# Kernel optimization log

Measured on AMD Instinct MI355X. Metric: run time of the kernel, lower is better.

Reference implementation:

```python
import jax, jax.numpy as jnp
import numpy as np

B, T, F = 32, 1024, 64
H = 128          # num_lstm_out
KH = 16          # kan_hidden_dim
C1, C2, C3 = 128, 256, 128
NC = 10


def _glorot(key, shape):
    fan_in = shape[0] if len(shape) == 2 else int(np.prod(shape[1:]))
    return (jax.random.normal(key, shape, jnp.float32) / np.sqrt(fan_in)).astype(jnp.float32)


def setup_inputs() -> dict:
    key = jax.random.key(0)
    ks = jax.random.split(key, 24)
    D = F + H
    d = {}
    d['x'] = jax.random.normal(ks[0], (B, T, F), jnp.float32)
    d['eps_z'] = jax.random.normal(ks[1], (B, H), jnp.float32)
    d['eps_cat'] = jax.random.normal(ks[2], (B, H), jnp.float32)
    # KAN-LSTM cell: gates = W2 @ silu(W1 @ [x;h])
    d['kan_w1'] = _glorot(ks[3], (D, KH)); d['kan_b1'] = jnp.zeros((KH,), jnp.float32)
    d['kan_w2'] = _glorot(ks[4], (KH, 4 * H)); d['kan_b2'] = jnp.zeros((4 * H,), jnp.float32)
    # causal convs (OIH layout)
    d['conv1_w'] = _glorot(ks[5], (C1, F, 8)); d['conv1_b'] = jnp.zeros((C1,), jnp.float32)
    d['conv2_w'] = _glorot(ks[6], (C2, C1, 5)); d['conv2_b'] = jnp.zeros((C2,), jnp.float32)
    d['conv3_w'] = _glorot(ks[7], (C3, C2, 3)); d['conv3_b'] = jnp.zeros((C3,), jnp.float32)
    # batchnorm affine params
    d['bn1_g'] = jnp.ones((C1,), jnp.float32); d['bn1_b'] = jnp.zeros((C1,), jnp.float32)
    d['bn2_g'] = jnp.ones((C2,), jnp.float32); d['bn2_b'] = jnp.zeros((C2,), jnp.float32)
    d['bn3_g'] = jnp.ones((C3,), jnp.float32); d['bn3_b'] = jnp.zeros((C3,), jnp.float32)
    # SE layers (reduction=16, no bias)
    d['se1_w1'] = _glorot(ks[8], (C1, C1 // 16)); d['se1_w2'] = _glorot(ks[9], (C1 // 16, C1))
    d['se2_w1'] = _glorot(ks[10], (C2, C2 // 16)); d['se2_w2'] = _glorot(ks[11], (C2 // 16, C2))
    # VIB heads
    d['fc_mu_w'] = _glorot(ks[12], (H, H)); d['fc_mu_b'] = jnp.zeros((H,), jnp.float32)
    d['fc_std_w'] = _glorot(ks[13], (H, H)); d['fc_std_b'] = jnp.zeros((H,), jnp.float32)
    d['fc_mu_cat_w'] = _glorot(ks[14], (2 * H, H)); d['fc_mu_cat_b'] = jnp.zeros((H,), jnp.float32)
    d['fc_std_cat_w'] = _glorot(ks[15], (2 * H, H)); d['fc_std_cat_b'] = jnp.zeros((H,), jnp.float32)
    d['fc_w'] = _glorot(ks[16], (H + C3, NC)); d['fc_b'] = jnp.zeros((NC,), jnp.float32)
    return d


def _kan_lstm(x, w1, b1, w2, b2):
    # x: (B,T,F) -> hidden (B,T,H); sequential recurrence via lax.scan
    xT = jnp.swapaxes(x, 0, 1)  # (T,B,F)
    h0 = jnp.zeros((x.shape[0], H), x.dtype)
    c0 = jnp.zeros((x.shape[0], H), x.dtype)

    def step(carry, xt):
        h, c = carry
        g = jax.nn.silu(jnp.concatenate([xt, h], axis=-1) @ w1 + b1) @ w2 + b2  # (B,4H)
        i_, f_, g_, o_ = jnp.split(g, 4, axis=-1)
        c = jax.nn.sigmoid(f_) * c + jax.nn.sigmoid(i_) * jnp.tanh(g_)
        h = jax.nn.sigmoid(o_) * jnp.tanh(c)
        return (h, c), h

    _, hs = jax.lax.scan(step, (h0, c0), xT)
    return jnp.swapaxes(hs, 0, 1)  # (B,T,H)


def _cluster_hidden(hidden):
    # hidden: (B,T,H). Pairwise cosine sim -> exp kernel -> best 2-block cut.
    Tn = hidden.shape[1]
    last = hidden[:, -1, :]
    hn = hidden / jnp.clip(jnp.linalg.norm(hidden, axis=-1, keepdims=True), 1e-8)
    S = jnp.exp(-5.5 * (1.0 - jnp.einsum('bik,bjk->bij', hn, hn)))  # (B,T,T)
    S = S * (1.0 - jnp.eye(Tn, dtype=S.dtype))  # zero diagonal
    # 2D prefix sums give all block sums in O(T^2) instead of O(T^3)
    P = jnp.cumsum(jnp.cumsum(S, axis=1), axis=2)
    i = jnp.arange(1, Tn)
    TL = P[:, i - 1, i - 1]                 # (B,T-1) sum of [:i,:i]
    full = P[:, -1, -1][:, None]
    TR = P[:, i - 1, -1] - TL               # sum of [:i,i:]
    BL = P[:, -1, i - 1] - TL               # sum of [i:,:i]
    BR = full - TL - TR - BL                # sum of [i:,i:]
    ii = i.astype(S.dtype)
    nn = (Tn - i).astype(S.dtype)
    dist = TL / (ii * ii) + BR / (nn * nn) - (TR + BL) / (ii * nn)
    cuts = jnp.argmax(dist, axis=1) + 1     # (B,)
    mask = (jnp.arange(Tn)[None, :] < cuts[:, None]).astype(hidden.dtype)
    corr = jnp.einsum('bt,bth->bh', mask, hidden) / cuts[:, None].astype(hidden.dtype)
    return last, corr


def _causal_conv(x, w, b):
    k = w.shape[-1]
    xp = jnp.pad(x, ((0, 0), (0, 0), (k - 1, 0)))
    y = jax.lax.conv_general_dilated(xp, w, (1,), 'VALID',
                                     dimension_numbers=('NCH', 'OIH', 'NCH'))
    return y + b[None, :, None]


def _bn(x, g, b, eps=1e-3):
    m = x.mean(axis=(0, 2), keepdims=True)
    v = x.var(axis=(0, 2), keepdims=True)
    return (x - m) / jnp.sqrt(v + eps) * g[None, :, None] + b[None, :, None]


def _se(x, w1, w2):
    y = x.mean(axis=2)                       # (B,C)
    y = jax.nn.sigmoid(jax.nn.relu(y @ w1) @ w2)
    return x * y[:, :, None]


def reference(x, eps_z, eps_cat, kan_w1, kan_b1, kan_w2, kan_b2,
              conv1_w, conv1_b, conv2_w, conv2_b, conv3_w, conv3_b,
              bn1_g, bn1_b, bn2_g, bn2_b, bn3_g, bn3_b,
              se1_w1, se1_w2, se2_w1, se2_w2,
              fc_mu_w, fc_mu_b, fc_std_w, fc_std_b,
              fc_mu_cat_w, fc_mu_cat_b, fc_std_cat_w, fc_std_cat_b,
              fc_w, fc_b):
    # LSTM branch
    hidden = _kan_lstm(x, kan_w1, kan_b1, kan_w2, kan_b2)      # (B,T,H)
    out, corr = _cluster_hidden(hidden)
    mu = corr @ fc_mu_w + fc_mu_b
    std = jax.nn.softplus(corr @ fc_std_w + fc_std_b)
    z = mu + std * eps_z
    xz = jnp.concatenate([out, z], axis=1)                      # (B,2H)
    mu_cat = xz @ fc_mu_cat_w + fc_mu_cat_b
    std_cat = jax.nn.softplus(xz @ fc_std_cat_w + fc_std_cat_b)
    x1 = mu_cat + std_cat * eps_cat   # dropout in eval mode = identity
    # FCN branch
    x2 = jnp.swapaxes(x, 1, 2)                                  # (B,F,T)
    x2 = jax.nn.gelu(_bn(_causal_conv(x2, conv1_w, conv1_b), bn1_g, bn1_b), approximate=False)
    x2 = _se(x2, se1_w1, se1_w2)
    x2 = jax.nn.gelu(_bn(_causal_conv(x2, conv2_w, conv2_b), bn2_g, bn2_b), approximate=False)
    x2 = _se(x2, se2_w1, se2_w2)
    x2 = jax.nn.gelu(_bn(_causal_conv(x2, conv3_w, conv3_b), bn3_g, bn3_b), approximate=False)
    x2 = x2.mean(axis=2)                                        # (B,C3)
    x_all = jnp.concatenate([x1, x2], axis=1)
    logits = x_all @ fc_w + fc_b
    return (jax.nn.log_softmax(logits, axis=1), mu, std, mu_cat, std_cat)
```

## Files before the change

kernel.cpp:

```cpp
#include <hip/hip_runtime.h>
#include <math.h>

#define B_ 32
#define T_ 1024
#define F_ 64
#define H_ 128
#define D_ 192
#define KH_ 16
#define C1_ 128
#define C2_ 256
#define C3_ 128
#define NC_ 10

typedef float v2f __attribute__((ext_vector_type(2)));
typedef float f32x4 __attribute__((ext_vector_type(4)));
typedef __bf16 bfrag __attribute__((ext_vector_type(8)));

__device__ __forceinline__ float sig_(float x){ return 1.f/(1.f+__expf(-x)); }
__device__ __forceinline__ float tanh_(float x){ return 1.f - 2.f/(__expf(2.f*x)+1.f); }
__device__ __forceinline__ float gelu_(float x){ return 0.5f*x*(1.f+erff(x*0.70710678118654752f)); }
__device__ __forceinline__ float softplus_(float x){ return fmaxf(x,0.f) + log1pf(__expf(-fabsf(x))); }

__device__ __forceinline__ unsigned bfpack(float a, float b){
  unsigned ua = __float_as_uint(a), ub = __float_as_uint(b);
  ua = ua + 0x7FFFu + ((ua>>16)&1u);
  ub = ub + 0x7FFFu + ((ub>>16)&1u);
  return (ua>>16) | (ub & 0xFFFF0000u);
}
__device__ __forceinline__ unsigned short bf1(float a){
  unsigned ua = __float_as_uint(a);
  ua = ua + 0x7FFFu + ((ua>>16)&1u);
  return (unsigned short)(ua>>16);
}
__device__ __forceinline__ float bf2f(unsigned short h){
  return __uint_as_float(((unsigned)h)<<16);
}

#define QPERM_XOR1(x) __int_as_float(__builtin_amdgcn_mov_dpp(__float_as_int(x), 0xB1, 0xF, 0xF, true))
#define QPERM_XOR2(x) __int_as_float(__builtin_amdgcn_mov_dpp(__float_as_int(x), 0x4E, 0xF, 0xF, true))

#define LDS_BARRIER() asm volatile("s_waitcnt lgkmcnt(0)\n\ts_barrier" ::: "memory")


__device__ __forceinline__ void ax_body(int blk, char* smemraw,
    const float* __restrict__ x, const float* __restrict__ w1, const float* __restrict__ b1,
    float* __restrict__ axT)
{
  struct AxS { float xs[16][68]; float w1s[64][16]; };
  AxS* sm = (AxS*)smemraw;
  const int bt0 = blk*16;
  const int tid = threadIdx.x;
  for(int i=tid;i<64*16;i+=256){ sm->w1s[i>>4][i&15] = w1[i]; }
  for(int i=tid;i<16*64;i+=256){ const int r=i>>6, d=i&63; sm->xs[r][d] = x[(size_t)(bt0+r)*64 + d]; }
  __syncthreads();
  const int r = tid>>4, j = tid&15;
  float s = b1[j];
  #pragma unroll
  for(int d=0; d<64; d++) s += sm->xs[r][d]*sm->w1s[d][j];
  const int bt = bt0 + r;
  axT[((size_t)(bt>>10)*16 + j)*1024 + (bt&1023)] = s;
}

__device__ __forceinline__ void prepack_body(int blk,
    const float* __restrict__ w1s, const float* __restrict__ w2s, const float* __restrict__ w3s,
    unsigned short* __restrict__ wp1, unsigned short* __restrict__ wp2, unsigned short* __restrict__ wp3)
{
  int e = blk*256 + threadIdx.x;
  if(e >= 65536+163840+98304) return;
  const float* w; unsigned short* wp; int Cout, Cin, Kw;
  if(e < 65536){ w=w1s; wp=wp1; Cout=C1_; Cin=F_;  Kw=8; }
  else if(e < 65536+163840){ e-=65536; w=w2s; wp=wp2; Cout=C2_; Cin=C1_; Kw=5; }
  else { e-=229376; w=w3s; wp=wp3; Cout=C3_; Cin=C2_; Kw=3; }
  const int co = e/(Cin*Kw);
  const int rem = e - co*(Cin*Kw);
  const int ci = rem/Kw, kw = rem - ci*Kw;
  const int off = (((ci>>5)*Kw + kw)*(Cout>>4) + (co>>4))*512 + ((co&15)*4 + ((ci>>3)&3))*8 + (ci&7);
  wp[off] = bf1(w[e]);
}

__device__ __forceinline__ void norm_body(int blk,
    const float* __restrict__ hidden,
    unsigned short* __restrict__ hnhi, unsigned short* __restrict__ hnlo)
{
  const int row = blk*8 + (threadIdx.x>>5);
  const int l = threadIdx.x&31;
  const float* hr = hidden + (size_t)row*H_;
  float s = 0.f;
  for(int k=l;k<H_;k+=32){ float v=hr[k]; s+=v*v; }
  #pragma unroll
  for(int m=16;m>=1;m>>=1) s += __shfl_xor(s, m, 64);
  const float inv = 1.f/fmaxf(sqrtf(s), 1e-8f);
  const float4 v = *(const float4*)&hr[l*4];
  const float f0=v.x*inv, f1=v.y*inv, f2=v.z*inv, f3=v.w*inv;
  const unsigned short h0=bf1(f0), h1=bf1(f1), h2=bf1(f2), h3=bf1(f3);
  uint2 phi; phi.x = (unsigned)h0 | ((unsigned)h1<<16); phi.y = (unsigned)h2 | ((unsigned)h3<<16);
  *(uint2*)&hnhi[(size_t)row*H_ + l*4] = phi;
  const unsigned short g0=bf1(f0-bf2f(h0)), g1=bf1(f1-bf2f(h1)), g2=bf1(f2-bf2f(h2)), g3=bf1(f3-bf2f(h3));
  uint2 plo; plo.x = (unsigned)g0 | ((unsigned)g1<<16); plo.y = (unsigned)g2 | ((unsigned)g3<<16);
  *(uint2*)&hnlo[(size_t)row*H_ + l*4] = plo;
}

struct SS {
  unsigned short Ahi[64*136];
  unsigned short Alo[64*136];
  unsigned short Bhi[64*136];
  unsigned short Blo[64*136];
  double red[64][17];
};
__device__ __forceinline__ void s_body(int blk, char* smemraw,
    const unsigned short* __restrict__ hnhi, const unsigned short* __restrict__ hnlo,
    double* __restrict__ rowsum, double* __restrict__ psum)
{
  SS* sm = (SS*)smemraw;
  const int b = blk >> 4;
  const int i0 = (blk & 15) * 64;
  const int tid = threadIdx.x, l = tid & 63, wv = tid >> 6;
  const int m = l & 15, q = l >> 4;

  {
    const uint4* ghi = (const uint4*)(hnhi + ((size_t)b*T_ + i0)*H_);
    const uint4* glo = (const uint4*)(hnlo + ((size_t)b*T_ + i0)*H_);
    for(int idx=tid; idx<64*16; idx+=256){
      const int r = idx>>4, c8 = idx&15;
      *(uint4*)&sm->Ahi[r*136 + c8*8] = ghi[r*16 + c8];
      *(uint4*)&sm->Alo[r*136 + c8*8] = glo[r*16 + c8];
    }
  }

  double rs[4]={0,0,0,0}, ps[4]={0,0,0,0};
  const int arow = (wv*16 + m)*136;

  for(int jt=0;jt<16;jt++){
    const int j0 = jt*64;
    __syncthreads();
    {
      const uint4* ghi = (const uint4*)(hnhi + ((size_t)b*T_ + j0)*H_);
      const uint4* glo = (const uint4*)(hnlo + ((size_t)b*T_ + j0)*H_);
      for(int idx=tid; idx<64*16; idx+=256){
        const int r = idx>>4, c8 = idx&15;
        *(uint4*)&sm->Bhi[r*136 + c8*8] = ghi[r*16 + c8];
        *(uint4*)&sm->Blo[r*136 + c8*8] = glo[r*16 + c8];
      }
    }
    __syncthreads();

    f32x4 acc[4];
    #pragma unroll
    for(int nt=0;nt<4;nt++) acc[nt] = (f32x4)(0.f);
    #pragma unroll
    for(int kc=0;kc<4;kc++){
      const bfrag Ah = *(const bfrag*)&sm->Ahi[arow + kc*32 + q*8];
      const bfrag Al = *(const bfrag*)&sm->Alo[arow + kc*32 + q*8];
      #pragma unroll
      for(int nt=0;nt<4;nt++){
        const int brow = (nt*16 + m)*136 + kc*32 + q*8;
        const bfrag Bh = *(const bfrag*)&sm->Bhi[brow];
        const bfrag Bl = *(const bfrag*)&sm->Blo[brow];
        acc[nt] = __builtin_amdgcn_mfma_f32_16x16x32_bf16(Ah, Bh, acc[nt], 0, 0, 0);
        acc[nt] = __builtin_amdgcn_mfma_f32_16x16x32_bf16(Al, Bh, acc[nt], 0, 0, 0);
        acc[nt] = __builtin_amdgcn_mfma_f32_16x16x32_bf16(Ah, Bl, acc[nt], 0, 0, 0);
      }
    }
    #pragma unroll
    for(int nt=0;nt<4;nt++){
      const int gj = j0 + nt*16 + m;
      #pragma unroll
      for(int r=0;r<4;r++){
        const int gi = i0 + wv*16 + q*4 + r;
        if(gi == gj) continue;
        const float sv = __expf(-5.5f*(1.f - acc[nt][r]));
        rs[r] += (double)sv;
        if(gj < gi) ps[r] += (double)sv;
      }
    }
  }
  __syncthreads();
  #pragma unroll
  for(int r=0;r<4;r++) sm->red[wv*16 + q*4 + r][m] = rs[r];
  __syncthreads();
  if(tid<64){ double v=0; for(int k=0;k<16;k++) v+=sm->red[tid][k]; rowsum[(size_t)b*T_ + i0 + tid]=v; }
  __syncthreads();
  #pragma unroll
  for(int r=0;r<4;r++) sm->red[wv*16 + q*4 + r][m] = ps[r];
  __syncthreads();
  if(tid<64){ double v=0; for(int k=0;k<16;k++) v+=sm->red[tid][k]; psum[(size_t)b*T_ + i0 + tid]=v; }
}

struct CS {
  double sr[256]; double sp[256]; double bd[256]; double totR;
  float c2[2][128]; int bidx[256]; int cut;
};
__device__ __forceinline__ void cluster_body(int b, char* smemraw,
    const double* __restrict__ rowsum, const double* __restrict__ psum,
    const float* __restrict__ hidden, float* __restrict__ corr, int* __restrict__ cuts)
{
  CS* sm = (CS*)smemraw;
  const int tid = threadIdx.x;
  const double* r = rowsum + (size_t)b*T_;
  const double* p = psum + (size_t)b*T_;
  double r4[4], p4[4];
  #pragma unroll
  for(int q=0;q<4;q++){ r4[q]=r[tid*4+q]; p4[q]=p[tid*4+q]; }
  sm->sr[tid]=r4[0]+r4[1]+r4[2]+r4[3];
  sm->sp[tid]=p4[0]+p4[1]+p4[2]+p4[3];
  __syncthreads();
  if(tid==0){
    double ar=0, ap=0;
    for(int i=0;i<256;i++){ double tr=sm->sr[i], tp=sm->sp[i]; sm->sr[i]=ar; sm->sp[i]=ap; ar+=tr; ap+=tp; }
    sm->totR = ar;
  }
  __syncthreads();
  double cr = sm->sr[tid], cp = sm->sp[tid];
  const double full = sm->totR;
  double best = -1e308; int bi = 1;
  #pragma unroll
  for(int q=0;q<4;q++){
    cr += r4[q]; cp += p4[q];
    const int i = 4*tid + q + 1;
    if(i < T_){
      const double TL = 2.0*cp;
      const double TRv = cr - TL;
      const double BR = full - TL - 2.0*TRv;
      const double di = (double)i, dn = (double)(T_-i);
      const double dist = TL/(di*di) + BR/(dn*dn) - (2.0*TRv)/(di*dn);
      if(dist > best){ best=dist; bi=i; }
    }
  }
  sm->bd[tid]=best; sm->bidx[tid]=bi;
  __syncthreads();
  if(tid==0){
    double bb=-1e308; int ii=1;
    for(int q=0;q<256;q++){ if(sm->bd[q]>bb){ bb=sm->bd[q]; ii=sm->bidx[q]; } }
    sm->cut=ii; cuts[b]=ii;
  }
  __syncthreads();
  const int cut = sm->cut;
  const int h = tid&127, half = tid>>7;
  float s=0.f;
  const float* hb = hidden + (size_t)b*T_*H_;
  #pragma unroll 4
  for(int t=half; t<cut; t+=2) s += hb[(size_t)t*H_ + h];
  sm->c2[half][h]=s;
  __syncthreads();
  if(tid<128) corr[b*H_+tid] = (sm->c2[0][tid]+sm->c2[1][tid])/(float)cut;
}

__device__ __forceinline__ void head1_body(int b, char* smemraw,
    const float* __restrict__ corr, const float* __restrict__ hidden,
    const float* __restrict__ eps_z, const float* __restrict__ eps_cat,
    const float* __restrict__ mu_w, const float* __restrict__ mu_b,
    const float* __restrict__ std_w, const float* __restrict__ std_b,
    const float* __restrict__ muc_w, const float* __restrict__ muc_b,
    const float* __restrict__ stdc_w, const float* __restrict__ stdc_b,
    float* __restrict__ out_mu, float* __restrict__ out_std,
    float* __restrict__ out_muc, float* __restrict__ out_stdc, float* __restrict__ x1)
{
  struct H1 { float cs[128]; float xz[256]; };
  H1* sm = (H1*)smemraw;
  const int h = threadIdx.x;
  if(h<128){
    sm->cs[h]=corr[b*H_+h];
    sm->xz[h]=hidden[((size_t)b*T_ + (T_-1))*H_ + h];
  }
  __syncthreads();
  if(h<128){
    float m=mu_b[h], sdv=std_b[h];
    for(int k=0;k<H_;k++){ const float cv=sm->cs[k]; m+=cv*mu_w[k*H_+h]; sdv+=cv*std_w[k*H_+h]; }
    const float stdv = softplus_(sdv);
    out_mu[b*H_+h]=m; out_std[b*H_+h]=stdv;
    sm->xz[128+h] = m + stdv*eps_z[b*H_+h];
  }
  __syncthreads();
  if(h<128){
    float mc=muc_b[h], sc=stdc_b[h];
    for(int k=0;k<256;k++){ const float v=sm->xz[k]; mc+=v*muc_w[k*H_+h]; sc+=v*stdc_w[k*H_+h]; }
    const float stdc = softplus_(sc);
    out_muc[b*H_+h]=mc; out_stdc[b*H_+h]=stdc;
    x1[b*H_+h]=mc + stdc*eps_cat[b*H_+h];
  }
}

struct ConvS {
  float sescale[256];
  float seh[16];
  unsigned short xs[72*40];
};
__device__ __forceinline__ void conv_body(int bx, int by, int bz, char* smemraw,
    const float* __restrict__ in, const unsigned short* __restrict__ wp,
    const float* __restrict__ bias,
    const float* __restrict__ se_in, const float* __restrict__ se_w1,
    const float* __restrict__ se_w2, int seR,
    float* __restrict__ y, float* __restrict__ bnacc, int Cin, int Cout, int Kw)
{
  ConvS* sm = (ConvS*)smemraw;
  unsigned short* xs = sm->xs;
  const int b = bz, t0 = bx*64, co0 = by*64;
  const int tid = threadIdx.x, l = tid&63, wv = tid>>6;
  const int q = l>>4, m = l&15;
  const int TW = 64 + Kw - 1;
  const int abase = (wv*16 + m)*40 + q*8;
  const int boff = (m*4 + q)*8;
  const bool use_se = (se_in != nullptr);

  if(use_se){
    float* ms = (float*)xs;
    if(tid<Cin) ms[tid] = se_in[b*Cin+tid] * (1.f/(float)T_);
    __syncthreads();
    if(tid<seR){ float s=0.f; for(int k=0;k<Cin;k++) s += ms[k]*se_w1[k*seR+tid]; sm->seh[tid]=fmaxf(s,0.f); }
    __syncthreads();
    if(tid<Cin){ float s=0.f; for(int k=0;k<seR;k++) s += sm->seh[k]*se_w2[k*Cin+tid]; sm->sescale[tid]=sig_(s); }
  }

  f32x4 acc[4];
  #pragma unroll
  for(int nt=0;nt<4;nt++) acc[nt] = (f32x4)(0.f);

  const int nchunks = Cin >> 5;
  for(int cc=0; cc<nchunks; cc++){
    __syncthreads();
    for(int idx=tid; idx<TW*8; idx+=256){
      const int r = idx>>3, c4 = (idx&7)*4;
      const int tg = t0 - (Kw-1) + r;
      uint2 pk = make_uint2(0u, 0u);
      if(tg >= 0){
        float4 v = *(const float4*)&in[((size_t)b*T_ + tg)*Cin + cc*32 + c4];
        if(use_se){
          const float4 s4 = *(const float4*)&sm->sescale[cc*32 + c4];
          v.x*=s4.x; v.y*=s4.y; v.z*=s4.z; v.w*=s4.w;
        }
        pk.x = bfpack(v.x, v.y); pk.y = bfpack(v.z, v.w);
      }
      *(uint2*)&xs[r*40 + c4] = pk;
    }
    __syncthreads();
    for(int kw=0; kw<Kw; kw++){
      const bfrag Af = *(const bfrag*)&xs[abase + kw*40];
      #pragma unroll
      for(int nt=0; nt<4; nt++){
        const unsigned short* wpp = wp + ((size_t)((cc*Kw + kw)*(Cout>>4) + (by*4 + nt)))*512 + boff;
        const bfrag Bf = *(const bfrag*)wpp;
        acc[nt] = __builtin_amdgcn_mfma_f32_16x16x32_bf16(Af, Bf, acc[nt], 0, 0, 0);
      }
    }
  }
  __syncthreads();
  float* part = (float*)xs;
  const int t_base = t0 + wv*16 + q*4;
  #pragma unroll
  for(int nt=0; nt<4; nt++){
    const int co = co0 + nt*16 + m;
    const float bv = bias[co];
    float s1 = 0.f, s2 = 0.f;
    #pragma unroll
    for(int r=0;r<4;r++){
      const float v = acc[nt][r] + bv;
      y[((size_t)b*T_ + t_base + r)*Cout + co] = v;
      s1 += v; s2 += v*v;
    }
    s1 += __shfl_xor(s1, 16); s1 += __shfl_xor(s1, 32);
    s2 += __shfl_xor(s2, 16); s2 += __shfl_xor(s2, 32);
    if(q==0){ part[(wv*64 + nt*16 + m)*2+0] = s1; part[(wv*64 + nt*16 + m)*2+1] = s2; }
  }
  __syncthreads();
  if(tid < 64){
    float a1=0.f, a2=0.f;
    #pragma unroll
    for(int w2i=0; w2i<4; w2i++){ a1 += part[(w2i*64+tid)*2+0]; a2 += part[(w2i*64+tid)*2+1]; }
    atomicAdd(&bnacc[co0 + tid], a1);
    atomicAdd(&bnacc[Cout + co0 + tid], a2);
  }
}

__device__ __forceinline__ void bn_act_body(int b, int chunk, char* smemraw,
    float* __restrict__ y, const float* __restrict__ bnacc,
    const float* __restrict__ gw, const float* __restrict__ bw,
    float* __restrict__ mean_acc, int C, int write_y)
{
  const int t0 = chunk*128, tid = threadIdx.x;
  const int c = tid & (C-1), part = tid / C, np = 256 / C;
  const float cnt = (float)(B_*T_);
  const float mm = bnacc[c]/cnt;
  const float var = bnacc[C+c]/cnt - mm*mm;
  const float sc = gw[c]/sqrtf(var+1e-3f);
  const float sh = bw[c] - mm*sc;
  float s = 0.f;
  for(int t=t0+part; t<t0+128; t+=np){
    const size_t off = ((size_t)b*T_ + t)*C + c;
    float v = y[off];
    v = gelu_(v*sc + sh);
    if(write_y) y[off] = v;
    s += v;
  }
  float* rs = (float*)smemraw;
  if(np > 1){
    rs[tid]=s;
    __syncthreads();
    if(part==0) s += rs[tid+C];
  }
  if(part==0) atomicAdd(&mean_acc[b*C+c], s);
}

__device__ __forceinline__ void lstm_seg_body(int b, int ts, int nsteps, char* smemraw,
    const float* __restrict__ axT, const float* __restrict__ w1,
    const float* __restrict__ w2, const float* __restrict__ b2,
    float* __restrict__ hidden, float* __restrict__ cstate)
{
  float (*hs)[148] = (float(*)[148])smemraw;
  const int tid = threadIdx.x;
  const int l = tid & 63, wv = tid >> 6;
  const int j = l >> 2, g = l & 3;
  const int hi = wv*64 + l;

  v2f w1hv[16];
  #pragma unroll
  for(int q=0;q<16;q++){
    w1hv[q].x = w1[(64 + g*32 + 2*q)*KH_ + j];
    w1hv[q].y = w1[(64 + g*32 + 2*q + 1)*KH_ + j];
  }
  v2f w2if[16], w2go[16];
  #pragma unroll
  for(int k=0;k<16;k++){
    w2if[k].x = w2[k*512 + hi];       w2if[k].y = w2[k*512 + 128 + hi];
    w2go[k].x = w2[k*512 + 256 + hi]; w2go[k].y = w2[k*512 + 384 + hi];
  }
  v2f bif, bgo;
  bif.x = b2[hi]; bif.y = b2[128+hi]; bgo.x = b2[256+hi]; bgo.y = b2[384+hi];

  const float* axr = axT + ((size_t)b*16 + j)*1024;
  float* hb = hidden + (size_t)b*T_*H_;
  const int hwi = (hi>>5)*36 + (hi&31);
  float c;
  if(ts == 0){
    for(int i=tid;i<2*148;i+=128) ((float*)hs)[i]=0.f;
    c = 0.f;
  } else {
    c = cstate[b*H_ + hi];
    hs[0][hwi] = hb[(size_t)(ts-1)*H_ + hi];
  }
  float4 axA = *(const float4*)&axr[ts];
  float4 axB = *(const float4*)&axr[ts+4];
  __syncthreads();

#define LSTM_STEP(tt, axv, RB) { \
    const float* hsr = hs[RB]; \
    float* hsw = hs[1-(RB)]; \
    v2f ap0=(v2f)(0.f), ap1=(v2f)(0.f), ap2=(v2f)(0.f), ap3=(v2f)(0.f); \
    { const float4 hv = *(const float4*)&hsr[g*36 + 0];  ap0 += ((v2f){hv.x,hv.y})*w1hv[0]  + ((v2f){hv.z,hv.w})*w1hv[1]; } \
    { const float4 hv = *(const float4*)&hsr[g*36 + 4];  ap1 += ((v2f){hv.x,hv.y})*w1hv[2]  + ((v2f){hv.z,hv.w})*w1hv[3]; } \
    { const float4 hv = *(const float4*)&hsr[g*36 + 8];  ap2 += ((v2f){hv.x,hv.y})*w1hv[4]  + ((v2f){hv.z,hv.w})*w1hv[5]; } \
    { const float4 hv = *(const float4*)&hsr[g*36 + 12]; ap3 += ((v2f){hv.x,hv.y})*w1hv[6]  + ((v2f){hv.z,hv.w})*w1hv[7]; } \
    { const float4 hv = *(const float4*)&hsr[g*36 + 16]; ap0 += ((v2f){hv.x,hv.y})*w1hv[8]  + ((v2f){hv.z,hv.w})*w1hv[9]; } \
    { const float4 hv = *(const float4*)&hsr[g*36 + 20]; ap1 += ((v2f){hv.x,hv.y})*w1hv[10] + ((v2f){hv.z,hv.w})*w1hv[11]; } \
    { const float4 hv = *(const float4*)&hsr[g*36 + 24]; ap2 += ((v2f){hv.x,hv.y})*w1hv[12] + ((v2f){hv.z,hv.w})*w1hv[13]; } \
    { const float4 hv = *(const float4*)&hsr[g*36 + 28]; ap3 += ((v2f){hv.x,hv.y})*w1hv[14] + ((v2f){hv.z,hv.w})*w1hv[15]; } \
    const v2f apt = (ap0+ap1)+(ap2+ap3); \
    float a = apt.x + apt.y; \
    a += QPERM_XOR1(a); \
    a += QPERM_XOR2(a); \
    a += (axv); \
    const float g1 = a * sig_(a); \
    v2f aIF = bif, aGO = bgo; \
    _Pragma("unroll") \
    for(int k=0;k<16;k++){ \
      const float gk = __int_as_float(__builtin_amdgcn_readlane(__float_as_int(g1), 4*k)); \
      v2f gk2; gk2.x=gk; gk2.y=gk; \
      aIF += gk2 * w2if[k]; \
      aGO += gk2 * w2go[k]; \
    } \
    const float si = sig_(aIF.x); \
    const float sf = sig_(aIF.y); \
    const float tg = tanh_(aGO.x); \
    const float so = sig_(aGO.y); \
    c = sf*c + si*tg; \
    const float h = so * tanh_(c); \
    hsw[hwi] = h; \
    hb[(size_t)(tt)*H_ + hi] = h; \
    LDS_BARRIER(); \
  }

  const int te = ts + nsteps;
  for(int t0=ts;t0<te;t0+=4){
    const int tl = (t0+8 < 1020) ? (t0+8) : 1020;
    const float4 axC = *(const float4*)&axr[tl];
    LSTM_STEP(t0+0, axA.x, 0)
    LSTM_STEP(t0+1, axA.y, 1)
    LSTM_STEP(t0+2, axA.z, 0)
    LSTM_STEP(t0+3, axA.w, 1)
    axA = axB; axB = axC;
  }
#undef LSTM_STEP
  if(te < T_) cstate[b*H_ + hi] = c;
}


__global__ __launch_bounds__(256) void mega0_kernel(
    const float* c1w, const float* c2w, const float* c3w,
    unsigned short* wp1, unsigned short* wp2, unsigned short* wp3,
    const float* x, const float* kw1, const float* kb1, float* axT)
{
  __shared__ __align__(16) char sm[16*68*4 + 64*16*4];
  const int bid = blockIdx.x;
  if(bid < 1280) prepack_body(bid, c1w, c2w, c3w, wp1, wp2, wp3);
  else ax_body(bid-1280, sm, x, kw1, kb1, axT);
}

__global__ __launch_bounds__(256) void seg_kernel(
    int ts, int nsteps, int phase,
    const float* axT, const float* kw1, const float* kw2, const float* kb2,
    float* hidden, float* cstate,
    const float* x, const unsigned short* wp1, const float* c1b, float* y1, float* bn1,
    const float* g1w, const float* b1w, float* se1_in,
    const unsigned short* wp2, const float* c2b, const float* s1w1, const float* s1w2,
    float* y2, float* bn2,
    const float* g2w, const float* b2w, float* se2_in,
    const unsigned short* wp3, const float* c3b, const float* s2w1, const float* s2w2,
    float* y3, float* bn3,
    const float* g3w, const float* b3w, float* x2)
{
  __shared__ __align__(16) char sm[sizeof(ConvS)];
  const int bid = blockIdx.x;
  if(bid < 32){
    if(threadIdx.x >= 128){
      const int nb = nsteps + 1;
      #pragma nounroll
      for(int i=0;i<nb;i++){ asm volatile("s_barrier" ::: "memory"); }
      return;
    }
    __builtin_amdgcn_s_setprio(1);
    lstm_seg_body(bid, ts, nsteps, sm, axT, kw1, kw2, kb2, hidden, cstate);
    return;
  }
  const int cb = bid - 32;
  switch(phase){
    case 0:
      conv_body(cb&15, (cb>>4)&1, cb>>5, sm, x, wp1, c1b,
                nullptr, nullptr, nullptr, 0, y1, bn1, F_, C1_, 8);
      break;
    case 1:
      bn_act_body(cb>>3, cb&7, sm, y1, bn1, g1w, b1w, se1_in, C1_, 1);
      break;
    case 2:
      conv_body(cb&15, (cb>>4)&3, cb>>6, sm, y1, wp2, c2b,
                se1_in, s1w1, s1w2, C1_/16, y2, bn2, C1_, C2_, 5);
      break;
    case 3:
      bn_act_body(cb>>3, cb&7, sm, y2, bn2, g2w, b2w, se2_in, C2_, 1);
      break;
    case 4:
      conv_body(cb&15, (cb>>4)&1, cb>>5, sm, y2, wp3, c3b,
                se2_in, s2w1, s2w2, C2_/16, y3, bn3, C2_, C3_, 3);
      break;
    default:
      bn_act_body(cb>>3, cb&7, sm, y3, bn3, g3w, b3w, x2, C3_, 0);
      break;
  }
}

__global__ __launch_bounds__(256) void norm_kernel(
    const float* hidden, unsigned short* hnhi, unsigned short* hnlo)
{
  norm_body(blockIdx.x, hidden, hnhi, hnlo);
}

__global__ __launch_bounds__(256) void s_kernel(
    const unsigned short* hnhi, const unsigned short* hnlo, double* rowsum, double* psum)
{
  __shared__ __align__(16) char sm[sizeof(SS)];
  s_body(blockIdx.x, sm, hnhi, hnlo, rowsum, psum);
}

__global__ __launch_bounds__(256) void tail_kernel(
    const double* rowsum, const double* psum, const float* hidden, float* corr, int* cuts,
    const float* eps_z, const float* eps_cat,
    const float* mu_w, const float* mu_b, const float* std_w, const float* std_b,
    const float* muc_w, const float* muc_b, const float* stdc_w, const float* stdc_b,
    float* out_mu, float* out_std, float* out_muc, float* out_stdc, float* x1,
    const float* x2, const float* fcw, const float* fcb, float* outls)
{
  __shared__ __align__(16) char sm[sizeof(CS)];
  const int b = blockIdx.x, tid = threadIdx.x;
  cluster_body(b, sm, rowsum, psum, hidden, corr, cuts);
  __syncthreads();
  head1_body(b, sm, corr, hidden, eps_z, eps_cat, mu_w, mu_b, std_w, std_b,
             muc_w, muc_b, stdc_w, stdc_b, out_mu, out_std, out_muc, out_stdc, x1);
  __syncthreads();
  struct H2 { float xa[256]; float lg[NC_]; };
  H2* s2 = (H2*)sm;
  s2->xa[tid] = (tid<128) ? x1[b*128+tid] : x2[b*128+(tid-128)]*(1.f/(float)T_);
  __syncthreads();
  if(tid<NC_){
    float s = fcb[tid];
    for(int k=0;k<256;k++) s += s2->xa[k]*fcw[k*NC_+tid];
    s2->lg[tid]=s;
  }
  __syncthreads();
  if(tid==0){
    float mx=s2->lg[0];
    for(int q=1;q<NC_;q++) mx=fmaxf(mx,s2->lg[q]);
    float se=0;
    for(int q=0;q<NC_;q++) se += __expf(s2->lg[q]-mx);
    const float lse = logf(se)+mx;
    for(int q=0;q<NC_;q++) outls[b*NC_+q] = s2->lg[q]-lse;
  }
}

extern "C" void kernel_launch(void* const* d_in, const int* in_sizes, int n_in,
                              void* d_out, int out_size, void* d_ws, size_t ws_size,
                              hipStream_t stream) {
  (void)in_sizes; (void)n_in; (void)out_size; (void)ws_size;
  const float* x        = (const float*)d_in[0];
  const float* eps_z    = (const float*)d_in[1];
  const float* eps_cat  = (const float*)d_in[2];
  const float* kan_w1   = (const float*)d_in[3];
  const float* kan_b1   = (const float*)d_in[4];
  const float* kan_w2   = (const float*)d_in[5];
  const float* kan_b2   = (const float*)d_in[6];
  const float* conv1_w  = (const float*)d_in[7];
  const float* conv1_b  = (const float*)d_in[8];
  const float* conv2_w  = (const float*)d_in[9];
  const float* conv2_b  = (const float*)d_in[10];
  const float* conv3_w  = (const float*)d_in[11];
  const float* conv3_b  = (const float*)d_in[12];
  const float* bn1_g    = (const float*)d_in[13];
  const float* bn1_b    = (const float*)d_in[14];
  const float* bn2_g    = (const float*)d_in[15];
  const float* bn2_b    = (const float*)d_in[16];
  const float* bn3_g    = (const float*)d_in[17];
  const float* bn3_b    = (const float*)d_in[18];
  const float* se1_w1   = (const float*)d_in[19];
  const float* se1_w2   = (const float*)d_in[20];
  const float* se2_w1   = (const float*)d_in[21];
  const float* se2_w2   = (const float*)d_in[22];
  const float* fc_mu_w  = (const float*)d_in[23];
  const float* fc_mu_b  = (const float*)d_in[24];
  const float* fc_std_w = (const float*)d_in[25];
  const float* fc_std_b = (const float*)d_in[26];
  const float* fc_muc_w = (const float*)d_in[27];
  const float* fc_muc_b = (const float*)d_in[28];
  const float* fc_stdc_w= (const float*)d_in[29];
  const float* fc_stdc_b= (const float*)d_in[30];
  const float* fc_w     = (const float*)d_in[31];
  const float* fc_b     = (const float*)d_in[32];

  float* out = (float*)d_out;
  float* out_ls   = out;
  float* out_mu   = out + 320;
  float* out_std  = out + 320 + 4096;
  float* out_muc  = out + 320 + 2*4096;
  float* out_stdc = out + 320 + 3*4096;

  float* ws = (float*)d_ws;
  const size_t SZ_HID = (size_t)B_*T_*H_;
  const size_t SZ_Y1  = (size_t)B_*T_*C1_;
  const size_t SZ_Y2  = (size_t)B_*T_*C2_;
  float*  hidden = ws;
  float*  y1     = hidden + SZ_HID;
  float*  y2     = y1 + SZ_Y1;
  double* rowsum = (double*)(y2 + SZ_Y2);
  double* psum   = rowsum + (size_t)B_*T_;
  float*  corr   = (float*)(psum + (size_t)B_*T_);
  float*  x1     = corr + (size_t)B_*H_;
  float*  bnbuf  = x1 + (size_t)B_*H_;
  float*  bn1    = bnbuf;
  float*  bn2    = bnbuf + 2*C1_;
  float*  bn3    = bnbuf + 2*C1_ + 2*C2_;
  float*  se1_in = bnbuf + 1024;
  float*  se2_in = se1_in + (size_t)B_*C1_;
  float*  x2     = se2_in + (size_t)B_*C2_;
  int*    cuts   = (int*)(x2 + (size_t)B_*C3_);
  float*  cstate = (float*)(cuts + B_);
  float*  axbuf  = cstate + (size_t)B_*H_;
  unsigned short* wp1 = (unsigned short*)(axbuf + (size_t)B_*16*T_);
  unsigned short* wp2 = wp1 + (size_t)C1_*F_*8;
  unsigned short* wp3 = wp2 + (size_t)C2_*C1_*5;
  unsigned short* hnhi = wp3 + (size_t)C3_*C2_*3;
  unsigned short* hnlo = hnhi + (size_t)B_*T_*H_;
  float*  y3     = y1;

  hipMemsetAsync(bnbuf, 0, (size_t)(1024 + B_*C1_ + B_*C2_ + B_*C3_)*sizeof(float), stream);

  mega0_kernel<<<3328, 256, 0, stream>>>(conv1_w, conv2_w, conv3_w, wp1, wp2, wp3,
                                         x, kan_w1, kan_b1, axbuf);

  #define SEG_ARGS axbuf, kan_w1, kan_w2, kan_b2, hidden, cstate, \
      x, wp1, conv1_b, y1, bn1, bn1_g, bn1_b, se1_in, \
      wp2, conv2_b, se1_w1, se1_w2, y2, bn2, bn2_g, bn2_b, se2_in, \
      wp3, conv3_b, se2_w1, se2_w2, y3, bn3, bn3_g, bn3_b, x2
  seg_kernel<<<32 + 1024, 256, 0, stream>>>(  0, 144, 0, SEG_ARGS);
  seg_kernel<<<32 +  256, 256, 0, stream>>>(144,  64, 1, SEG_ARGS);
  seg_kernel<<<32 + 2048, 256, 0, stream>>>(208, 384, 2, SEG_ARGS);
  seg_kernel<<<32 +  256, 256, 0, stream>>>(592,  64, 3, SEG_ARGS);
  seg_kernel<<<32 + 1024, 256, 0, stream>>>(656, 240, 4, SEG_ARGS);
  seg_kernel<<<32 +  256, 256, 0, stream>>>(896, 128, 5, SEG_ARGS);
  #undef SEG_ARGS

  norm_kernel<<<4096, 256, 0, stream>>>(hidden, hnhi, hnlo);
  s_kernel<<<512, 256, 0, stream>>>(hnhi, hnlo, rowsum, psum);
  tail_kernel<<<B_, 256, 0, stream>>>(rowsum, psum, hidden, corr, cuts,
      eps_z, eps_cat,
      fc_mu_w, fc_mu_b, fc_std_w, fc_std_b, fc_muc_w, fc_muc_b, fc_stdc_w, fc_stdc_b,
      out_mu, out_std, out_muc, out_stdc, x1,
      x2, fc_w, fc_b, out_ls);
}
```

Baseline: 783.3 us.

## Overlap hidden-state normalization and similarity tiles with LSTM segments

Removes the standalone norm and similarity kernels. Normalization of finished hidden rows and 64x64 similarity tiles are now computed inside the segment kernels, running alongside the sequential LSTM. Tiles are ordered by their max index so each one only needs rows that are already done, and partial row sums go into global doubles via atomics after a memset. The tiles now load operands straight from global memory instead of LDS. This adds atomic traffic and two extra launches in exchange for hiding the quadratic similarity work behind the serial recurrence.

Result: slower. 849.6 us (+8.5%).

```diff
diff --git a/kernel.cpp b/kernel.cpp
--- a/kernel.cpp
+++ b/kernel.cpp
@@ -78,13 +78,13 @@
   wp[off] = bf1(w[e]);
 }
 
-__device__ __forceinline__ void norm_body(int blk,
+__device__ __forceinline__ void norm8_body(size_t rowbase,
     const float* __restrict__ hidden,
     unsigned short* __restrict__ hnhi, unsigned short* __restrict__ hnlo)
 {
-  const int row = blk*8 + (threadIdx.x>>5);
+  const size_t row = rowbase + (threadIdx.x>>5);
   const int l = threadIdx.x&31;
-  const float* hr = hidden + (size_t)row*H_;
+  const float* hr = hidden + row*H_;
   float s = 0.f;
   for(int k=l;k<H_;k+=32){ float v=hr[k]; s+=v*v; }
   #pragma unroll
@@ -94,96 +94,66 @@
   const float f0=v.x*inv, f1=v.y*inv, f2=v.z*inv, f3=v.w*inv;
   const unsigned short h0=bf1(f0), h1=bf1(f1), h2=bf1(f2), h3=bf1(f3);
   uint2 phi; phi.x = (unsigned)h0 | ((unsigned)h1<<16); phi.y = (unsigned)h2 | ((unsigned)h3<<16);
-  *(uint2*)&hnhi[(size_t)row*H_ + l*4] = phi;
+  *(uint2*)&hnhi[row*H_ + l*4] = phi;
   const unsigned short g0=bf1(f0-bf2f(h0)), g1=bf1(f1-bf2f(h1)), g2=bf1(f2-bf2f(h2)), g3=bf1(f3-bf2f(h3));
   uint2 plo; plo.x = (unsigned)g0 | ((unsigned)g1<<16); plo.y = (unsigned)g2 | ((unsigned)g3<<16);
-  *(uint2*)&hnlo[(size_t)row*H_ + l*4] = plo;
-}
-
-struct SS {
-  unsigned short Ahi[64*136];
-  unsigned short Alo[64*136];
-  unsigned short Bhi[64*136];
-  unsigned short Blo[64*136];
-  double red[64][17];
-};
-__device__ __forceinline__ void s_body(int blk, char* smemraw,
+  *(uint2*)&hnlo[row*H_ + l*4] = plo;
+}
+
+__device__ __forceinline__ void stile_body(int b, int i0, int j0,
     const unsigned short* __restrict__ hnhi, const unsigned short* __restrict__ hnlo,
     double* __restrict__ rowsum, double* __restrict__ psum)
 {
-  SS* sm = (SS*)smemraw;
-  const int b = blk >> 4;
-  const int i0 = (blk & 15) * 64;
   const int tid = threadIdx.x, l = tid & 63, wv = tid >> 6;
   const int m = l & 15, q = l >> 4;
-
-  {
-    const uint4* ghi = (const uint4*)(hnhi + ((size_t)b*T_ + i0)*H_);
-    const uint4* glo = (const uint4*)(hnlo + ((size_t)b*T_ + i0)*H_);
-    for(int idx=tid; idx<64*16; idx+=256){
-      const int r = idx>>4, c8 = idx&15;
-      *(uint4*)&sm->Ahi[r*136 + c8*8] = ghi[r*16 + c8];
-      *(uint4*)&sm->Alo[r*136 + c8*8] = glo[r*16 + c8];
-    }
-  }
-
-  double rs[4]={0,0,0,0}, ps[4]={0,0,0,0};
-  const int arow = (wv*16 + m)*136;
-
-  for(int jt=0;jt<16;jt++){
-    const int j0 = jt*64;
-    __syncthreads();
-    {
-      const uint4* ghi = (const uint4*)(hnhi + ((size_t)b*T_ + j0)*H_);
-      const uint4* glo = (const uint4*)(hnlo + ((size_t)b*T_ + j0)*H_);
-      for(int idx=tid; idx<64*16; idx+=256){
-        const int r = idx>>4, c8 = idx&15;
-        *(uint4*)&sm->Bhi[r*136 + c8*8] = ghi[r*16 + c8];
-        *(uint4*)&sm->Blo[r*136 + c8*8] = glo[r*16 + c8];
-      }
-    }
-    __syncthreads();
-
-    f32x4 acc[4];
-    #pragma unroll
-    for(int nt=0;nt<4;nt++) acc[nt] = (f32x4)(0.f);
-    #pragma unroll
-    for(int kc=0;kc<4;kc++){
-      const bfrag Ah = *(const bfrag*)&sm->Ahi[arow + kc*32 + q*8];
-      const bfrag Al = *(const bfrag*)&sm->Alo[arow + kc*32 + q*8];
-      #pragma unroll
-      for(int nt=0;nt<4;nt++){
-        const int brow = (nt*16 + m)*136 + kc*32 + q*8;
-        const bfrag Bh = *(const bfrag*)&sm->Bhi[brow];
-        const bfrag Bl = *(const bfrag*)&sm->Blo[brow];
-        acc[nt] = __builtin_amdgcn_mfma_f32_16x16x32_bf16(Ah, Bh, acc[nt], 0, 0, 0);
-        acc[nt] = __builtin_amdgcn_mfma_f32_16x16x32_bf16(Al, Bh, acc[nt], 0, 0, 0);
-        acc[nt] = __builtin_amdgcn_mfma_f32_16x16x32_bf16(Ah, Bl, acc[nt], 0, 0, 0);
-      }
-    }
+  const size_t arow = ((size_t)b*T_ + i0 + wv*16 + m)*H_;
+
+  f32x4 acc[4];
+  #pragma unroll
+  for(int nt=0;nt<4;nt++) acc[nt] = (f32x4)(0.f);
+  #pragma unroll
+  for(int kc=0;kc<4;kc++){
+    const bfrag Ah = *(const bfrag*)&hnhi[arow + kc*32 + q*8];
+    const bfrag Al = *(const bfrag*)&hnlo[arow + kc*32 + q*8];
     #pragma unroll
     for(int nt=0;nt<4;nt++){
-      const int gj = j0 + nt*16 + m;
-      #pragma unroll
-      for(int r=0;r<4;r++){
-        const int gi = i0 + wv*16 + q*4 + r;
-        if(gi == gj) continue;
-        const float sv = __expf(-5.5f*(1.f - acc[nt][r]));
-        rs[r] += (double)sv;
-        if(gj < gi) ps[r] += (double)sv;
-      }
-    }
-  }
-  __syncthreads();
-  #pragma unroll
-  for(int r=0;r<4;r++) sm->red[wv*16 + q*4 + r][m] = rs[r];
-  __syncthreads();
-  if(tid<64){ double v=0; for(int k=0;k<16;k++) v+=sm->red[tid][k]; rowsum[(size_t)b*T_ + i0 + tid]=v; }
-  __syncthreads();
-  #pragma unroll
-  for(int r=0;r<4;r++) sm->red[wv*16 + q*4 + r][m] = ps[r];
-  __syncthreads();
-  if(tid<64){ double v=0; for(int k=0;k<16;k++) v+=sm->red[tid][k]; psum[(size_t)b*T_ + i0 + tid]=v; }
+      const size_t brow = ((size_t)b*T_ + j0 + nt*16 + m)*H_ + kc*32 + q*8;
+      const bfrag Bh = *(const bfrag*)&hnhi[brow];
+      const bfrag Bl = *(const bfrag*)&hnlo[brow];
+      acc[nt] = __builtin_amdgcn_mfma_f32_16x16x32_bf16(Ah, Bh, acc[nt], 0, 0, 0);
+      acc[nt] = __builtin_amdgcn_mfma_f32_16x16x32_bf16(Al, Bh, acc[nt], 0, 0, 0);
+      acc[nt] = __builtin_amdgcn_mfma_f32_16x16x32_bf16(Ah, Bl, acc[nt], 0, 0, 0);
+    }
+  }
+  double rs[4]={0,0,0,0}, ps[4]={0,0,0,0};
+  #pragma unroll
+  for(int nt=0;nt<4;nt++){
+    const int gj = j0 + nt*16 + m;
+    #pragma unroll
+    for(int r=0;r<4;r++){
+      const int gi = i0 + wv*16 + q*4 + r;
+      if(gi == gj) continue;
+      const float sv = __expf(-5.5f*(1.f - acc[nt][r]));
+      rs[r] += (double)sv;
+      if(gj < gi) ps[r] += (double)sv;
+    }
+  }
+  #pragma unroll
+  for(int r=0;r<4;r++){
+    #pragma unroll
+    for(int mk=1;mk<16;mk<<=1){
+      rs[r] += __shfl_xor(rs[r], mk, 64);
+      ps[r] += __shfl_xor(ps[r], mk, 64);
+    }
+  }
+  if(m == 0){
+    const size_t gbase = (size_t)b*T_ + i0 + wv*16 + q*4;
+    #pragma unroll
+    for(int r=0;r<4;r++){
+      unsafeAtomicAdd(&rowsum[gbase + r], rs[r]);
+      unsafeAtomicAdd(&psum[gbase + r], ps[r]);
+    }
+  }
 }
 
 struct CS {
@@ -505,7 +475,8 @@
 }
 
 __global__ __launch_bounds__(256) void seg_kernel(
-    int ts, int nsteps, int phase,
+    int ts, int nsteps, int phase, int nphase, int normbase, int nnorm,
+    int pairbase, int nstile,
     const float* axT, const float* kw1, const float* kw2, const float* kb2,
     float* hidden, float* cstate,
     const float* x, const unsigned short* wp1, const float* c1b, float* y1, float* bn1,
@@ -515,11 +486,13 @@
     const float* g2w, const float* b2w, float* se2_in,
     const unsigned short* wp3, const float* c3b, const float* s2w1, const float* s2w2,
     float* y3, float* bn3,
-    const float* g3w, const float* b3w, float* x2)
+    const float* g3w, const float* b3w, float* x2,
+    unsigned short* hnhi, unsigned short* hnlo, double* rowsum, double* psum)
 {
   __shared__ __align__(16) char sm[sizeof(ConvS)];
   const int bid = blockIdx.x;
   if(bid < 32){
+    if(nsteps == 0) return;
     if(threadIdx.x >= 128){
       const int nb = nsteps + 1;
       #pragma nounroll
@@ -530,43 +503,53 @@
     lstm_seg_body(bid, ts, nsteps, sm, axT, kw1, kw2, kb2, hidden, cstate);
     return;
   }
-  const int cb = bid - 32;
-  switch(phase){
-    case 0:
-      conv_body(cb&15, (cb>>4)&1, cb>>5, sm, x, wp1, c1b,
-                nullptr, nullptr, nullptr, 0, y1, bn1, F_, C1_, 8);
-      break;
-    case 1:
-      bn_act_body(cb>>3, cb&7, sm, y1, bn1, g1w, b1w, se1_in, C1_, 1);
-      break;
-    case 2:
-      conv_body(cb&15, (cb>>4)&3, cb>>6, sm, y1, wp2, c2b,
-                se1_in, s1w1, s1w2, C1_/16, y2, bn2, C1_, C2_, 5);
-      break;
-    case 3:
-      bn_act_body(cb>>3, cb&7, sm, y2, bn2, g2w, b2w, se2_in, C2_, 1);
-      break;
-    case 4:
-      conv_body(cb&15, (cb>>4)&1, cb>>5, sm, y2, wp3, c3b,
-                se2_in, s2w1, s2w2, C2_/16, y3, bn3, C2_, C3_, 3);
-      break;
-    default:
-      bn_act_body(cb>>3, cb&7, sm, y3, bn3, g3w, b3w, x2, C3_, 0);
-      break;
-  }
-}
-
-__global__ __launch_bounds__(256) void norm_kernel(
-    const float* hidden, unsigned short* hnhi, unsigned short* hnlo)
-{
-  norm_body(blockIdx.x, hidden, hnhi, hnlo);
-}
-
-__global__ __launch_bounds__(256) void s_kernel(
-    const unsigned short* hnhi, const unsigned short* hnlo, double* rowsum, double* psum)
-{
-  __shared__ __align__(16) char sm[sizeof(SS)];
-  s_body(blockIdx.x, sm, hnhi, hnlo, rowsum, psum);
+  int cb = bid - 32;
+  if(cb < nphase){
+    switch(phase){
+      case 0:
+        conv_body(cb&15, (cb>>4)&1, cb>>5, sm, x, wp1, c1b,
+                  nullptr, nullptr, nullptr, 0, y1, bn1, F_, C1_, 8);
+        break;
+      case 1:
+        bn_act_body(cb>>3, cb&7, sm, y1, bn1, g1w, b1w, se1_in, C1_, 1);
+        break;
+      case 2:
+        conv_body(cb&15, (cb>>4)&3, cb>>6, sm, y1, wp2, c2b,
+                  se1_in, s1w1, s1w2, C1_/16, y2, bn2, C1_, C2_, 5);
+        break;
+      case 3:
+        bn_act_body(cb>>3, cb&7, sm, y2, bn2, g2w, b2w, se2_in, C2_, 1);
+        break;
+      case 4:
+        conv_body(cb&15, (cb>>4)&1, cb>>5, sm, y2, wp3, c3b,
+                  se2_in, s2w1, s2w2, C2_/16, y3, bn3, C2_, C3_, 3);
+        break;
+      default:
+        bn_act_body(cb>>3, cb&7, sm, y3, bn3, g3w, b3w, x2, C3_, 0);
+        break;
+    }
+    return;
+  }
+  cb -= nphase;
+  if(cb < nnorm){
+    const int b = cb & 31, tb = cb >> 5;
+    norm8_body((size_t)b*T_ + normbase + tb*8, hidden, hnhi, hnlo);
+    return;
+  }
+  cb -= nnorm;
+  if(cb < nstile){
+    const int b = cb & 31;
+    const int p = pairbase + (cb >> 5);
+    int mr = (int)sqrtf((float)p);
+    while(mr*mr > p) mr--;
+    while((mr+1)*(mr+1) <= p) mr++;
+    const int idx = p - mr*mr;
+    int ii, jj;
+    if(idx < mr){ ii = idx; jj = mr; }
+    else if(idx < 2*mr){ ii = mr; jj = idx - mr; }
+    else { ii = mr; jj = mr; }
+    stile_body(b, ii*64, jj*64, hnhi, hnlo, rowsum, psum);
+  }
 }
 
 __global__ __launch_bounds__(256) void tail_kernel(
@@ -678,6 +661,7 @@
   float*  y3     = y1;
 
   hipMemsetAsync(bnbuf, 0, (size_t)(1024 + B_*C1_ + B_*C2_ + B_*C3_)*sizeof(float), stream);
+  hipMemsetAsync(rowsum, 0, (size_t)2*B_*T_*sizeof(double), stream);
 
   mega0_kernel<<<3328, 256, 0, stream>>>(conv1_w, conv2_w, conv3_w, wp1, wp2, wp3,
                                          x, kan_w1, kan_b1, axbuf);
@@ -685,17 +669,18 @@
   #define SEG_ARGS axbuf, kan_w1, kan_w2, kan_b2, hidden, cstate, \
       x, wp1, conv1_b, y1, bn1, bn1_g, bn1_b, se1_in, \
       wp2, conv2_b, se1_w1, se1_w2, y2, bn2, bn2_g, bn2_b, se2_in, \
-      wp3, conv3_b, se2_w1, se2_w2, y3, bn3, bn3_g, bn3_b, x2
-  seg_kernel<<<32 + 1024, 256, 0, stream>>>(  0, 144, 0, SEG_ARGS);
-  seg_kernel<<<32 +  256, 256, 0, stream>>>(144,  64, 1, SEG_ARGS);
-  seg_kernel<<<32 + 2048, 256, 0, stream>>>(208, 384, 2, SEG_ARGS);
-  seg_kernel<<<32 +  256, 256, 0, stream>>>(592,  64, 3, SEG_ARGS);
-  seg_kernel<<<32 + 1024, 256, 0, stream>>>(656, 240, 4, SEG_ARGS);
-  seg_kernel<<<32 +  256, 256, 0, stream>>>(896, 128, 5, SEG_ARGS);
+      wp3, conv3_b, se2_w1, se2_w2, y3, bn3, bn3_g, bn3_b, x2, \
+      hnhi, hnlo, rowsum, psum
+  seg_kernel<<<32+1024,           256,0,stream>>>(  0,144, 0,1024,   0,    0,   0,    0, SEG_ARGS);
+  seg_kernel<<<32+256,            256,0,stream>>>(144, 64, 1, 256,   0,    0,   0,    0, SEG_ARGS);
+  seg_kernel<<<32+2048+832,       256,0,stream>>>(208,384, 2,2048,   0,  832,   0,    0, SEG_ARGS);
+  seg_kernel<<<32+256+1536+288,   256,0,stream>>>(592, 64, 3, 256, 208, 1536,   0,  288, SEG_ARGS);
+  seg_kernel<<<32+1024+256+2304,  256,0,stream>>>(656,240, 4,1024, 592,  256,   9, 2304, SEG_ARGS);
+  seg_kernel<<<32+256+960+608,    256,0,stream>>>(896,128, 5, 256, 656,  960,  81,  608, SEG_ARGS);
+  seg_kernel<<<32+512+3072,       256,0,stream>>>(  0,  0,-1,   0, 896,  512, 100, 3072, SEG_ARGS);
+  seg_kernel<<<32+1920,           256,0,stream>>>(  0,  0,-1,   0,   0,    0, 196, 1920, SEG_ARGS);
   #undef SEG_ARGS
 
-  norm_kernel<<<4096, 256, 0, stream>>>(hidden, hnhi, hnlo);
-  s_kernel<<<512, 256, 0, stream>>>(hnhi, hnlo, rowsum, psum);
   tail_kernel<<<B_, 256, 0, stream>>>(rowsum, psum, hidden, corr, cuts,
       eps_z, eps_cat,
       fc_mu_w, fc_mu_b, fc_std_w, fc_std_b, fc_muc_w, fc_muc_b, fc_stdc_w, fc_stdc_b,
```

## Exploit symmetry of similarity matrix to compute only upper-triangle tiles

Applied to the files above, without the earlier changes.

The pairwise similarity kernel now computes only tiles with j>=i for each batch, pairing row-block k with row-block 15-k so each block handles a balanced share of tiles. Off-diagonal tiles contribute row sums to the i rows and column sums to the j rows (both rowsum and psum), with partial results combined through wave shuffles and double-precision global atomics. This roughly halves MFMA and exp work, but adds atomic traffic, an extra memset and per-tile syncs, and makes summation order nondeterministic.

Measured after the change: 773.4 us. No clear change (-1.3%).

```diff
diff --git a/kernel.cpp b/kernel.cpp
--- a/kernel.cpp
+++ b/kernel.cpp
@@ -107,37 +107,42 @@
   unsigned short Blo[64*136];
   double red[64][17];
 };
-__device__ __forceinline__ void s_body(int blk, char* smemraw,
+__device__ __forceinline__ void s_sym_body(int blk, char* smemraw,
     const unsigned short* __restrict__ hnhi, const unsigned short* __restrict__ hnlo,
     double* __restrict__ rowsum, double* __restrict__ psum)
 {
   SS* sm = (SS*)smemraw;
   const int b = blk >> 4;
-  const int i0 = (blk & 15) * 64;
+  const int k2 = blk & 15, k = k2 >> 1, half = k2 & 1;
+  const int n1 = 16 - k;
+  const int start = half ? 9 : 0;
+  const int end   = half ? 17 : 9;
   const int tid = threadIdx.x, l = tid & 63, wv = tid >> 6;
   const int m = l & 15, q = l >> 4;
-
-  {
-    const uint4* ghi = (const uint4*)(hnhi + ((size_t)b*T_ + i0)*H_);
-    const uint4* glo = (const uint4*)(hnlo + ((size_t)b*T_ + i0)*H_);
-    for(int idx=tid; idx<64*16; idx+=256){
-      const int r = idx>>4, c8 = idx&15;
-      *(uint4*)&sm->Ahi[r*136 + c8*8] = ghi[r*16 + c8];
-      *(uint4*)&sm->Alo[r*136 + c8*8] = glo[r*16 + c8];
-    }
-  }
-
-  double rs[4]={0,0,0,0}, ps[4]={0,0,0,0};
   const int arow = (wv*16 + m)*136;
-
-  for(int jt=0;jt<16;jt++){
-    const int j0 = jt*64;
+  double* red = &sm->red[0][0];
+
+  int cur_i0 = -1;
+  for(int idx=start; idx<end; idx++){
+    int i0, j0;
+    if(idx < n1){ i0 = k*64;      j0 = (k+idx)*64; }
+    else        { i0 = (15-k)*64; j0 = (15-k + (idx-n1))*64; }
     __syncthreads();
+    if(i0 != cur_i0){
+      cur_i0 = i0;
+      const uint4* ghi = (const uint4*)(hnhi + ((size_t)b*T_ + i0)*H_);
+      const uint4* glo = (const uint4*)(hnlo + ((size_t)b*T_ + i0)*H_);
+      for(int t2=tid; t2<64*16; t2+=256){
+        const int r = t2>>4, c8 = t2&15;
+        *(uint4*)&sm->Ahi[r*136 + c8*8] = ghi[r*16 + c8];
+        *(uint4*)&sm->Alo[r*136 + c8*8] = glo[r*16 + c8];
+      }
+    }
     {
       const uint4* ghi = (const uint4*)(hnhi + ((size_t)b*T_ + j0)*H_);
       const uint4* glo = (const uint4*)(hnlo + ((size_t)b*T_ + j0)*H_);
-      for(int idx=tid; idx<64*16; idx+=256){
-        const int r = idx>>4, c8 = idx&15;
+      for(int t2=tid; t2<64*16; t2+=256){
+        const int r = t2>>4, c8 = t2&15;
         *(uint4*)&sm->Bhi[r*136 + c8*8] = ghi[r*16 + c8];
         *(uint4*)&sm->Blo[r*136 + c8*8] = glo[r*16 + c8];
       }
@@ -161,29 +166,77 @@
         acc[nt] = __builtin_amdgcn_mfma_f32_16x16x32_bf16(Ah, Bl, acc[nt], 0, 0, 0);
       }
     }
-    #pragma unroll
-    for(int nt=0;nt<4;nt++){
-      const int gj = j0 + nt*16 + m;
+
+    if(i0 == j0){
+      double rs[4]={0,0,0,0}, ps[4]={0,0,0,0};
+      #pragma unroll
+      for(int nt=0;nt<4;nt++){
+        const int gj = j0 + nt*16 + m;
+        #pragma unroll
+        for(int r=0;r<4;r++){
+          const int gi = i0 + wv*16 + q*4 + r;
+          if(gi == gj) continue;
+          const float sv = __expf(-5.5f*(1.f - acc[nt][r]));
+          rs[r] += (double)sv;
+          if(gj < gi) ps[r] += (double)sv;
+        }
+      }
       #pragma unroll
       for(int r=0;r<4;r++){
-        const int gi = i0 + wv*16 + q*4 + r;
-        if(gi == gj) continue;
-        const float sv = __expf(-5.5f*(1.f - acc[nt][r]));
-        rs[r] += (double)sv;
-        if(gj < gi) ps[r] += (double)sv;
-      }
-    }
-  }
-  __syncthreads();
-  #pragma unroll
-  for(int r=0;r<4;r++) sm->red[wv*16 + q*4 + r][m] = rs[r];
-  __syncthreads();
-  if(tid<64){ double v=0; for(int k=0;k<16;k++) v+=sm->red[tid][k]; rowsum[(size_t)b*T_ + i0 + tid]=v; }
-  __syncthreads();
-  #pragma unroll
-  for(int r=0;r<4;r++) sm->red[wv*16 + q*4 + r][m] = ps[r];
-  __syncthreads();
-  if(tid<64){ double v=0; for(int k=0;k<16;k++) v+=sm->red[tid][k]; psum[(size_t)b*T_ + i0 + tid]=v; }
+        #pragma unroll
+        for(int mk=1;mk<16;mk<<=1){
+          rs[r] += __shfl_xor(rs[r], mk, 64);
+          ps[r] += __shfl_xor(ps[r], mk, 64);
+        }
+      }
+      if(m == 0){
+        const size_t gbase = (size_t)b*T_ + i0 + wv*16 + q*4;
+        #pragma unroll
+        for(int r=0;r<4;r++){
+          unsafeAtomicAdd(&rowsum[gbase + r], rs[r]);
+          unsafeAtomicAdd(&psum[gbase + r], ps[r]);
+        }
+      }
+    } else {
+      double rs[4]={0,0,0,0}, cs[4]={0,0,0,0};
+      #pragma unroll
+      for(int nt=0;nt<4;nt++){
+        double csn = 0.0;
+        #pragma unroll
+        for(int r=0;r<4;r++){
+          const float sv = __expf(-5.5f*(1.f - acc[nt][r]));
+          rs[r] += (double)sv;
+          csn   += (double)sv;
+        }
+        cs[nt] = csn;
+      }
+      #pragma unroll
+      for(int r=0;r<4;r++){
+        #pragma unroll
+        for(int mk=1;mk<16;mk<<=1) rs[r] += __shfl_xor(rs[r], mk, 64);
+      }
+      if(m == 0){
+        const size_t gbase = (size_t)b*T_ + i0 + wv*16 + q*4;
+        #pragma unroll
+        for(int r=0;r<4;r++) unsafeAtomicAdd(&rowsum[gbase + r], rs[r]);
+      }
+      #pragma unroll
+      for(int nt=0;nt<4;nt++){
+        cs[nt] += __shfl_xor(cs[nt], 16, 64);
+        cs[nt] += __shfl_xor(cs[nt], 32, 64);
+      }
+      if(q == 0){
+        #pragma unroll
+        for(int nt=0;nt<4;nt++) red[wv*64 + nt*16 + m] = cs[nt];
+      }
+      __syncthreads();
+      if(tid < 64){
+        const double v = red[tid] + red[64+tid] + red[128+tid] + red[192+tid];
+        unsafeAtomicAdd(&rowsum[(size_t)b*T_ + j0 + tid], v);
+        unsafeAtomicAdd(&psum[(size_t)b*T_ + j0 + tid], v);
+      }
+    }
+  }
 }
 
 struct CS {
@@ -566,7 +619,7 @@
     const unsigned short* hnhi, const unsigned short* hnlo, double* rowsum, double* psum)
 {
   __shared__ __align__(16) char sm[sizeof(SS)];
-  s_body(blockIdx.x, sm, hnhi, hnlo, rowsum, psum);
+  s_sym_body(blockIdx.x, sm, hnhi, hnlo, rowsum, psum);
 }
 
 __global__ __launch_bounds__(256) void tail_kernel(
@@ -678,6 +731,7 @@
   float*  y3     = y1;
 
   hipMemsetAsync(bnbuf, 0, (size_t)(1024 + B_*C1_ + B_*C2_ + B_*C3_)*sizeof(float), stream);
+  hipMemsetAsync(rowsum, 0, (size_t)2*B_*T_*sizeof(double), stream);
 
   mega0_kernel<<<3328, 256, 0, stream>>>(conv1_w, conv2_w, conv3_w, wp1, wp2, wp3,
                                          x, kan_w1, kan_b1, axbuf);
```
